# Kernel optimization log

Hardware: AMD Instinct MI355X
Metric: run time of the kernel (lower is better)

The kernel has to match this reference:

```python
import jax, jax.numpy as jnp
import numpy as np

BS, S, N, C, H, CP, T, CT, NB = 1, 2, 2048, 128, 8, 16, 512, 384, 3
DH = C // H
INF = 1.0e8

def _ln(x, w, b, eps=1e-5):
    mu = jnp.mean(x, axis=-1, keepdims=True)
    var = jnp.var(x, axis=-1, keepdims=True)
    return (x - mu) * jax.lax.rsqrt(var + eps) * w + b

def _ln_na(x, eps=1e-5):
    mu = jnp.mean(x, axis=-1, keepdims=True)
    var = jnp.var(x, axis=-1, keepdims=True)
    return (x - mu) * jax.lax.rsqrt(var + eps)

def _betas(n):
    # query row l belongs to window centered at 32*(l//32)+16; keys within +/- n_keys//2=64
    l = jnp.arange(n)
    centers = (l // 32) * 32 + 16
    m = jnp.arange(n)
    ok = (m[None, :] >= (centers - 64)[:, None]) & (m[None, :] < (centers + 64)[:, None])
    return jnp.where(ok, 0.0, -INF).astype(jnp.float32)

def setup_inputs():
    key = jax.random.key(0)
    ks = iter(jax.random.split(key, 80))
    def W(*shape):
        return jax.random.normal(next(ks), shape, dtype=jnp.float32) * 0.05
    return {
        "atom_single": jax.random.normal(next(ks), (BS, S, N, C), dtype=jnp.float32),
        "atom_proj": jax.random.normal(next(ks), (BS, N, C), dtype=jnp.float32),
        "atom_pair": jax.random.normal(next(ks), (BS, N, N, CP), dtype=jnp.float32),
        "mask": jnp.ones((BS, N), jnp.float32),
        "tok_idx": jnp.sort(jax.random.randint(next(ks), (BS, N), 0, T), axis=-1),
        "aln_s_w": jnp.ones((NB, C), jnp.float32), "aln_s_b": jnp.zeros((NB, C), jnp.float32),
        "aln_gate_w": W(NB, C, C), "aln_gate_b": jnp.zeros((NB, C), jnp.float32),
        "aln_shift_w": W(NB, C, C),
        "q_w": W(NB, C, C), "q_b": jnp.zeros((NB, C), jnp.float32),
        "k_w": W(NB, C, C), "v_w": W(NB, C, C),
        "pair_ln_w": jnp.ones((NB, CP), jnp.float32), "pair_ln_b": jnp.zeros((NB, CP), jnp.float32),
        "pair_w": W(NB, CP, H),
        "gate_w": W(NB, C, C), "out_w": W(NB, C, C),
        "og_w": W(NB, C, C), "og_b": jnp.full((NB, C), -2.0, jnp.float32),
        "t_aln_s_w": jnp.ones((NB, C), jnp.float32), "t_aln_s_b": jnp.zeros((NB, C), jnp.float32),
        "t_aln_gate_w": W(NB, C, C), "t_aln_gate_b": jnp.zeros((NB, C), jnp.float32),
        "t_aln_shift_w": W(NB, C, C),
        "t_a_w": W(NB, C, 2 * C), "t_b_w": W(NB, C, 2 * C),
        "t_out_w": W(NB, 2 * C, C),
        "t_og_w": W(NB, C, C), "t_og_b": jnp.full((NB, C), -2.0, jnp.float32),
        "tok_w": W(C, CT),
    }

def _forward(atom_single, atom_proj, atom_pair, mask, tok_idx, aln_s_w, aln_s_b, aln_gate_w, aln_gate_b, aln_shift_w, q_w, q_b, k_w, v_w, pair_ln_w, pair_ln_b, pair_w, gate_w, out_w, og_w, og_b, t_aln_s_w, t_aln_s_b, t_aln_gate_w, t_aln_gate_b, t_aln_shift_w, t_a_w, t_b_w, t_out_w, t_og_w, t_og_b, tok_w):
    betas = _betas(N)[None, None, None]                        # [1,1,1,N,N]
    mask_bias = ((mask - 1.0) * INF)[:, None, None, None, :]   # [bs,1,1,1,N]
    s = atom_proj[:, None]                                     # [bs,1,N,C]
    a = atom_single                                            # [bs,S,N,C]
    for i in range(NB):
        # AttentionPairBias with AdaLN conditioning on s
        sn = _ln(s, aln_s_w[i], aln_s_b[i])
        a1 = jax.nn.sigmoid(sn @ aln_gate_w[i] + aln_gate_b[i]) * _ln_na(a) + sn @ aln_shift_w[i]
        q = (a1 @ q_w[i] + q_b[i]).reshape(BS, S, N, H, DH)
        k = (a1 @ k_w[i]).reshape(BS, S, N, H, DH)
        v = (a1 @ v_w[i]).reshape(BS, S, N, H, DH)
        zb = _ln(atom_pair, pair_ln_w[i], pair_ln_b[i]) @ pair_w[i]    # [bs,N,N,H]
        zb = jnp.transpose(zb, (0, 3, 1, 2))[:, None]                  # [bs,1,H,N,N]
        logits = jnp.einsum('bsqhd,bskhd->bshqk', q, k) / np.float32(np.sqrt(DH)) + zb + betas + mask_bias
        p = jax.nn.softmax(logits, axis=-1)
        o = jnp.einsum('bshqk,bskhd->bsqhd', p, v).reshape(BS, S, N, C)
        o = (jax.nn.sigmoid(a1 @ gate_w[i]) * o) @ out_w[i]
        a = a + jax.nn.sigmoid(sn @ og_w[i] + og_b[i]) * o
        # ConditionedTransitionBlock (SwiGLU with adaLN-Zero gating)
        sn2 = _ln(s, t_aln_s_w[i], t_aln_s_b[i])
        a2 = jax.nn.sigmoid(sn2 @ t_aln_gate_w[i] + t_aln_gate_b[i]) * _ln_na(a) + sn2 @ t_aln_shift_w[i]
        hidden = jax.nn.silu(a2 @ t_a_w[i]) * (a2 @ t_b_w[i])
        a = a + jax.nn.sigmoid(sn2 @ t_og_w[i] + t_og_b[i]) * (hidden @ t_out_w[i])
    # project to token dim, relu, scatter-mean atoms -> tokens
    q_tok = jax.nn.relu(a @ tok_w)                             # [bs,S,N,CT]
    oh = jax.nn.one_hot(tok_idx, T, dtype=q_tok.dtype)         # [bs,N,T]
    cnt = jnp.clip(jnp.sum(oh, axis=1), 1.0)                   # [bs,T]
    tok = jnp.einsum('bsnc,bnt->bstc', q_tok, oh) / cnt[:, None, :, None]
    return tok

def reference(atom_single, atom_proj, atom_pair, mask, tok_idx, aln_s_w, aln_s_b, aln_gate_w, aln_gate_b, aln_shift_w, q_w, q_b, k_w, v_w, pair_ln_w, pair_ln_b, pair_w, gate_w, out_w, og_w, og_b, t_aln_s_w, t_aln_s_b, t_aln_gate_w, t_aln_gate_b, t_aln_shift_w, t_a_w, t_b_w, t_out_w, t_og_w, t_og_b, tok_w):
    return _forward(atom_single, atom_proj, atom_pair, mask, tok_idx, aln_s_w, aln_s_b, aln_gate_w, aln_gate_b, aln_shift_w, q_w, q_b, k_w, v_w, pair_ln_w, pair_ln_b, pair_w, gate_w, out_w, og_w, og_b, t_aln_s_w, t_aln_s_b, t_aln_gate_w, t_aln_gate_b, t_aln_shift_w, t_a_w, t_b_w, t_out_w, t_og_w, t_og_b, tok_w)
```

## Files before the change

kernel.cpp:

```cpp
#include <hip/hip_runtime.h>
#include <math.h>

#define NATOM 2048
#define CD 128
#define SD 2
#define TT 512
#define CTD 384
#define NBI 3
#define MR 4096

typedef unsigned short ushortx;
typedef __attribute__((ext_vector_type(8))) short bf16x8;
typedef __attribute__((ext_vector_type(4))) float f32x4;

__device__ __forceinline__ float sigm(float x){ return 1.0f/(1.0f+expf(-x)); }
__device__ __forceinline__ ushortx f2b(float f){
  union { float f; unsigned u; } v; v.f = f;
  unsigned r = v.u + 0x7fffu + ((v.u>>16)&1u);
  return (ushortx)(r>>16);
}
union U8 { ushortx u[8]; float4 v; };

#define OFFB_W3T    0ll
#define OFFB_B3     589824ll
#define OFFB_WQKVGT 599040ll
#define OFFB_BQ     992256ll
#define OFFB_WOUTT  998400ll
#define OFFB_WABT   1096704ll
#define OFFB_WTOUTT 1489920ll
#define OFFB_WTOKT  1686528ll
#define OFFB_A1     4930560ll
#define OFFB_SNP    9124864ll
#define OFFB_A      27999232ll
#define OFFB_QKVG   30096384ll
#define OFFB_ZB     38484992ll
#define OFFB_QTOK   63650816ll

struct WPtrs {
  const float *aln_gate_w, *aln_gate_b, *aln_shift_w, *og_w, *og_b;
  const float *t_aln_gate_w, *t_aln_gate_b, *t_aln_shift_w, *t_og_w, *t_og_b;
  const float *q_w, *q_b, *k_w, *v_w, *gate_w, *out_w;
  const float *t_a_w, *t_b_w, *t_out_w, *tok_w;
};

__global__ __launch_bounds__(256) void pack_kernel(WPtrs P, char* __restrict__ wsb)
{
  long long idx = (long long)blockIdx.x*256 + threadIdx.x;
  const long long s0=294912, s1=2304, s2=196608, s3=1536, s4=49152, s5=196608, s6=98304, s7=49152;
  if (idx < s0) {
    int which = (int)(idx/49152); int r = (int)(idx%49152); int n=r/128, k=r%128;
    int i = which>>1, t = which&1;
    const float* src;
    if (n<128)      src = (t?P.t_aln_gate_w :P.aln_gate_w ) + i*16384 + k*128 + n;
    else if (n<256) src = (t?P.t_aln_shift_w:P.aln_shift_w) + i*16384 + k*128 + (n-128);
    else            src = (t?P.t_og_w       :P.og_w       ) + i*16384 + k*128 + (n-256);
    ((ushortx*)(wsb+OFFB_W3T))[idx] = f2b(*src); return;
  }
  idx -= s0;
  if (idx < s1) {
    int which = (int)(idx/384); int col = (int)(idx%384); int i=which>>1, t=which&1;
    float v = 0.f;
    if (col<128)       v = (t?P.t_aln_gate_b:P.aln_gate_b)[i*128+col];
    else if (col>=256) v = (t?P.t_og_b      :P.og_b      )[i*128+col-256];
    ((float*)(wsb+OFFB_B3))[idx] = v; return;
  }
  idx -= s1;
  if (idx < s2) {
    int i = (int)(idx/65536); int r = (int)(idx%65536); int n=r/128, k=r%128;
    int seg = n>>7, c = n&127;
    const float* src = (seg==0?P.q_w: seg==1?P.k_w: seg==2?P.v_w: P.gate_w) + i*16384 + k*128 + c;
    ((ushortx*)(wsb+OFFB_WQKVGT))[idx] = f2b(*src); return;
  }
  idx -= s2;
  if (idx < s3) {
    int i = (int)(idx/512); int col = (int)(idx%512);
    ((float*)(wsb+OFFB_BQ))[idx] = (col<128) ? P.q_b[i*128+col] : 0.f; return;
  }
  idx -= s3;
  if (idx < s4) {
    int i = (int)(idx/16384); int r = (int)(idx%16384); int n=r/128, k=r%128;
    ((ushortx*)(wsb+OFFB_WOUTT))[idx] = f2b(P.out_w[i*16384 + k*128 + n]); return;
  }
  idx -= s4;
  if (idx < s5) {
    int i = (int)(idx/65536); int r = (int)(idx%65536); int n=r/128, k=r%128;
    const float* src = (n<256) ? P.t_a_w + i*32768 + k*256 + n
                               : P.t_b_w + i*32768 + k*256 + (n-256);
    ((ushortx*)(wsb+OFFB_WABT))[idx] = f2b(*src); return;
  }
  idx -= s5;
  if (idx < s6) {
    int i = (int)(idx/32768); int r = (int)(idx%32768); int n=r/256, k=r%256;
    ((ushortx*)(wsb+OFFB_WTOUTT))[idx] = f2b(P.t_out_w[i*32768 + k*128 + n]); return;
  }
  idx -= s6;
  if (idx < s7) {
    int n = (int)(idx/128); int k = (int)(idx%128);
    ((ushortx*)(wsb+OFFB_WTOKT))[idx] = f2b(P.tok_w[k*384 + n]); return;
  }
}

__global__ __launch_bounds__(256) void copy_f(const float* __restrict__ src, float* __restrict__ dst, int n){
  int i = blockIdx.x*256 + threadIdx.x;
  if (i<n) dst[i] = src[i];
}

__global__ __launch_bounds__(256) void zb_kernel(const float* __restrict__ atom_pair,
  const float* __restrict__ plw, const float* __restrict__ plb, const float* __restrict__ pw,
  float* __restrict__ zb)
{
  int idx = blockIdx.x*256 + threadIdx.x;
  int q = idx>>7, j = idx&127;
  int m = (q & ~31) - 48 + j;
  bool ok = (m>=0 && m<NATOM);
  float x[16]; float mu=0.f, rs=0.f;
  if (ok){
    float s=0.f, sq=0.f;
    const float* p = atom_pair + ((long long)q*NATOM + m)*16;
    #pragma unroll
    for (int c=0;c<16;c++){ x[c]=p[c]; s+=x[c]; sq+=x[c]*x[c]; }
    mu = s*(1.f/16.f); float var = sq*(1.f/16.f)-mu*mu; rs = rsqrtf(var+1e-5f);
  }
  #pragma unroll
  for (int it=0; it<NBI; it++){
    float out[8] = {0,0,0,0,0,0,0,0};
    if (ok){
      #pragma unroll
      for (int c=0;c<16;c++){
        float xn = (x[c]-mu)*rs*plw[it*16+c] + plb[it*16+c];
        #pragma unroll
        for (int h=0;h<8;h++) out[h] += xn * pw[it*128 + c*8 + h];
      }
    }
    #pragma unroll
    for (int h=0;h<8;h++)
      zb[(((long long)it*8+h)*NATOM + q)*128 + j] = out[h];
  }
}

__global__ __launch_bounds__(256) void attn_kernel(const float* __restrict__ qkvg,
  const float* __restrict__ zb, const float* __restrict__ mask, ushortx* __restrict__ og)
{
  int qb = blockIdx.x, h = blockIdx.y, s = blockIdx.z;
  int base = qb*32 - 48;
  __shared__ float Qs[32][20], Ks[128][20], Vs[128][20], Ls[32][132], maskb[128];
  __shared__ float redx[32][8], rowv[32];
  int tid = threadIdx.x;
  for (int idx=tid; idx<32*4; idx+=256){
    int r=idx>>2, d4=(idx&3)*4;
    *(float4*)&Qs[r][d4] = *(const float4*)&qkvg[((long long)(s*NATOM + qb*32 + r))*512 + h*16 + d4];
  }
  for (int idx=tid; idx<128*4; idx+=256){
    int j=idx>>2, d4=(idx&3)*4;
    int m = base + j; int mc = m<0?0:(m>NATOM-1?NATOM-1:m);
    long long row = ((long long)(s*NATOM + mc))*512;
    *(float4*)&Ks[j][d4] = *(const float4*)&qkvg[row + 128 + h*16 + d4];
    *(float4*)&Vs[j][d4] = *(const float4*)&qkvg[row + 256 + h*16 + d4];
  }
  if (tid < 128){
    int m = base + tid;
    maskb[tid] = (m>=0 && m<NATOM) ? (mask[m]-1.0f)*1e8f : -1e30f;
  }
  __syncthreads();
  int r = tid>>3, g = tid&7;
  {
    float4 q0=*(float4*)&Qs[r][0], q1=*(float4*)&Qs[r][4], q2=*(float4*)&Qs[r][8], q3=*(float4*)&Qs[r][12];
    const float* zrow = zb + ((long long)h*NATOM + (qb*32+r))*128;
    #pragma unroll
    for (int j=g; j<128; j+=8){
      float4 k0=*(float4*)&Ks[j][0], k1=*(float4*)&Ks[j][4], k2=*(float4*)&Ks[j][8], k3=*(float4*)&Ks[j][12];
      float dot = q0.x*k0.x + q0.y*k0.y + q0.z*k0.z + q0.w*k0.w
                + q1.x*k1.x + q1.y*k1.y + q1.z*k1.z + q1.w*k1.w
                + q2.x*k2.x + q2.y*k2.y + q2.z*k2.z + q2.w*k2.w
                + q3.x*k3.x + q3.y*k3.y + q3.z*k3.z + q3.w*k3.w;
      Ls[r][j] = dot*0.25f + zrow[j] + maskb[j];
    }
  }
  __syncthreads();
  float pmax = -1e30f;
  for (int j=g*16; j<g*16+16; j++) pmax = fmaxf(pmax, Ls[r][j]);
  redx[r][g] = pmax; __syncthreads();
  if (g==0){ float mx=redx[r][0]; for(int u=1;u<8;u++) mx=fmaxf(mx,redx[r][u]); rowv[r]=mx; }
  __syncthreads();
  float mx = rowv[r];
  float psum = 0.f;
  for (int j=g*16; j<g*16+16; j++){ float e = expf(Ls[r][j]-mx); Ls[r][j]=e; psum += e; }
  redx[r][g] = psum; __syncthreads();
  if (g==0){ float sm=0.f; for(int u=0;u<8;u++) sm+=redx[r][u]; rowv[r]=sm; }
  __syncthreads();
  {
    int q2=tid>>3, dg=(tid>>1)&3, jh=tid&1;
    float4 acc = make_float4(0.f,0.f,0.f,0.f);
    for (int j=jh*64; j<jh*64+64; j++){
      float p = Ls[q2][j];
      float4 v = *(float4*)&Vs[j][dg*4];
      acc.x += p*v.x; acc.y += p*v.y; acc.z += p*v.z; acc.w += p*v.w;
    }
    acc.x += __shfl_xor(acc.x,1); acc.y += __shfl_xor(acc.y,1);
    acc.z += __shfl_xor(acc.z,1); acc.w += __shfl_xor(acc.w,1);
    if (jh==0){
      long long mrow = (long long)(s*NATOM + qb*32 + q2);
      float inv = 1.0f / rowv[q2];
      float4 gt = *(const float4*)&qkvg[mrow*512 + 384 + h*16 + dg*4];
      ushortx* op = og + mrow*128 + h*16 + dg*4;
      op[0] = f2b(sigm(gt.x)*acc.x*inv);
      op[1] = f2b(sigm(gt.y)*acc.y*inv);
      op[2] = f2b(sigm(gt.z)*acc.z*inv);
      op[3] = f2b(sigm(gt.w)*acc.w*inv);
    }
  }
}

template<int AM>
__global__ __launch_bounds__(256) void gemm_f(
    const void* __restrict__ Asrc, long long strideA,
    const ushortx* __restrict__ B, long long strideB,
    const float* __restrict__ bias, long long strideBias,
    float* C, long long strideC,
    int M, int N, int K, int mode,
    const float* __restrict__ gate, int gate_ld, int gate_coloff,
    const float* __restrict__ p1, const float* __restrict__ p2,
    const float* __restrict__ p3, const float* __restrict__ p4)
{
  int z = blockIdx.z;
  B += z*strideB; C += z*strideC;
  if (bias) bias += z*strideBias;
  __shared__ ushortx At[64][136];
  __shared__ ushortx Bt[64][136];
  int tid = threadIdx.x;
  int rowBase = blockIdx.y*64, colBase = blockIdx.x*64;
  int wave = tid>>6, lane = tid&63;
  int wr = (wave>>1)*32, wc = (wave&1)*32;
  int lr = lane&15, lk = (lane>>4)*8;
  f32x4 acc[2][2];
  #pragma unroll
  for (int i=0;i<2;i++)
    #pragma unroll
    for (int j=0;j<2;j++) acc[i][j] = (f32x4){0.f,0.f,0.f,0.f};

  int sr = tid>>2, q = tid&3, cs = q*32;
  int row = rowBase + sr;

  for (int kc=0; kc<K; kc+=128){
    if (kc) __syncthreads();
    if (AM==0){
      const ushortx* Ab = (const ushortx*)Asrc + z*strideA;
      const float4* ag = (const float4*)(Ab + (long long)row*K + kc + cs);
      #pragma unroll
      for (int u=0;u<4;u++) *(float4*)&At[sr][cs+u*8] = ag[u];
    } else if (AM==3){
      const float* Af_ = (const float*)Asrc;
      const float4* ar = (const float4*)(Af_ + (long long)row*128 + cs);
      #pragma unroll
      for (int u=0;u<4;u++){
        float4 a = ar[2*u], b = ar[2*u+1];
        U8 pk;
        pk.u[0]=f2b(a.x); pk.u[1]=f2b(a.y); pk.u[2]=f2b(a.z); pk.u[3]=f2b(a.w);
        pk.u[4]=f2b(b.x); pk.u[5]=f2b(b.y); pk.u[6]=f2b(b.z); pk.u[7]=f2b(b.w);
        *(float4*)&At[sr][cs+u*8] = pk.v;
      }
    } else if (AM==2){
      const float* hp = (const float*)Asrc;
      const float4* xr = (const float4*)(hp + (long long)row*512 + kc + cs);
      const float4* yr = (const float4*)(hp + (long long)row*512 + 256 + kc + cs);
      #pragma unroll
      for (int u=0;u<4;u++){
        float4 xa = xr[2*u], xb = xr[2*u+1];
        float4 ya = yr[2*u], yb = yr[2*u+1];
        U8 pk;
        pk.u[0]=f2b(xa.x*sigm(xa.x)*ya.x); pk.u[1]=f2b(xa.y*sigm(xa.y)*ya.y);
        pk.u[2]=f2b(xa.z*sigm(xa.z)*ya.z); pk.u[3]=f2b(xa.w*sigm(xa.w)*ya.w);
        pk.u[4]=f2b(xb.x*sigm(xb.x)*yb.x); pk.u[5]=f2b(xb.y*sigm(xb.y)*yb.y);
        pk.u[6]=f2b(xb.z*sigm(xb.z)*yb.z); pk.u[7]=f2b(xb.w*sigm(xb.w)*yb.w);
        *(float4*)&At[sr][cs+u*8] = pk.v;
      }
    } else {
      const float* arow = (AM==4) ? ((const float*)Asrc + (long long)row*128)
                                  : ((const float*)Asrc + (long long)row*128);
      float x[32]; float s=0.f, sq=0.f;
      const float4* ar = (const float4*)(arow + cs);
      #pragma unroll
      for (int u=0;u<8;u++){
        float4 t = ar[u];
        x[4*u]=t.x; x[4*u+1]=t.y; x[4*u+2]=t.z; x[4*u+3]=t.w;
        s += t.x+t.y+t.z+t.w;
        sq += t.x*t.x+t.y*t.y+t.z*t.z+t.w*t.w;
      }
      s += __shfl_xor(s,1); s += __shfl_xor(s,2);
      sq += __shfl_xor(sq,1); sq += __shfl_xor(sq,2);
      float mu = s*(1.f/128.f), var = sq*(1.f/128.f)-mu*mu;
      float rs = rsqrtf(var + 1e-5f);
      if (AM==1){
        const float* sp = p1 + (long long)(row & (NATOM-1))*384;
        const float4* gr = (const float4*)(sp + cs);
        const float4* hr = (const float4*)(sp + 128 + cs);
        #pragma unroll
        for (int u=0;u<4;u++){
          float4 ga = gr[2*u], gb = gr[2*u+1];
          float4 ha = hr[2*u], hb = hr[2*u+1];
          U8 pk;
          pk.u[0]=f2b(sigm(ga.x)*((x[8*u  ]-mu)*rs)+ha.x);
          pk.u[1]=f2b(sigm(ga.y)*((x[8*u+1]-mu)*rs)+ha.y);
          pk.u[2]=f2b(sigm(ga.z)*((x[8*u+2]-mu)*rs)+ha.z);
          pk.u[3]=f2b(sigm(ga.w)*((x[8*u+3]-mu)*rs)+ha.w);
          pk.u[4]=f2b(sigm(gb.x)*((x[8*u+4]-mu)*rs)+hb.x);
          pk.u[5]=f2b(sigm(gb.y)*((x[8*u+5]-mu)*rs)+hb.y);
          pk.u[6]=f2b(sigm(gb.z)*((x[8*u+6]-mu)*rs)+hb.z);
          pk.u[7]=f2b(sigm(gb.w)*((x[8*u+7]-mu)*rs)+hb.w);
          *(float4*)&At[sr][cs+u*8] = pk.v;
        }
      } else {
        int iw = z>>1, tw = z&1;
        const float* w = (tw?p3:p1) + iw*128;
        const float* b = (tw?p4:p2) + iw*128;
        const float4* wrp = (const float4*)(w + cs);
        const float4* brp = (const float4*)(b + cs);
        #pragma unroll
        for (int u=0;u<4;u++){
          float4 wa = wrp[2*u], wb = wrp[2*u+1];
          float4 ba = brp[2*u], bb = brp[2*u+1];
          U8 pk;
          pk.u[0]=f2b((x[8*u  ]-mu)*rs*wa.x+ba.x);
          pk.u[1]=f2b((x[8*u+1]-mu)*rs*wa.y+ba.y);
          pk.u[2]=f2b((x[8*u+2]-mu)*rs*wa.z+ba.z);
          pk.u[3]=f2b((x[8*u+3]-mu)*rs*wa.w+ba.w);
          pk.u[4]=f2b((x[8*u+4]-mu)*rs*wb.x+bb.x);
          pk.u[5]=f2b((x[8*u+5]-mu)*rs*wb.y+bb.y);
          pk.u[6]=f2b((x[8*u+6]-mu)*rs*wb.z+bb.z);
          pk.u[7]=f2b((x[8*u+7]-mu)*rs*wb.w+bb.w);
          *(float4*)&At[sr][cs+u*8] = pk.v;
        }
      }
    }
    {
      const float4* bg = (const float4*)(B + (long long)(colBase+sr)*K + kc + cs);
      #pragma unroll
      for (int u=0;u<4;u++) *(float4*)&Bt[sr][cs+u*8] = bg[u];
    }
    __syncthreads();
    #pragma unroll
    for (int ks=0; ks<4; ks++){
      bf16x8 a0 = *(const bf16x8*)&At[wr+lr][ks*32+lk];
      bf16x8 a1 = *(const bf16x8*)&At[wr+16+lr][ks*32+lk];
      bf16x8 b0 = *(const bf16x8*)&Bt[wc+lr][ks*32+lk];
      bf16x8 b1 = *(const bf16x8*)&Bt[wc+16+lr][ks*32+lk];
      acc[0][0] = __builtin_amdgcn_mfma_f32_16x16x32_bf16(a0,b0,acc[0][0],0,0,0);
      acc[0][1] = __builtin_amdgcn_mfma_f32_16x16x32_bf16(a0,b1,acc[0][1],0,0,0);
      acc[1][0] = __builtin_amdgcn_mfma_f32_16x16x32_bf16(a1,b0,acc[1][0],0,0,0);
      acc[1][1] = __builtin_amdgcn_mfma_f32_16x16x32_bf16(a1,b1,acc[1][1],0,0,0);
    }
  }
  int crow0 = rowBase + wr + (lane>>4)*4;
  int ccol0 = colBase + wc + lr;
  #pragma unroll
  for (int i=0;i<2;i++){
    #pragma unroll
    for (int j=0;j<2;j++){
      int col = ccol0 + j*16;
      float bv = bias ? bias[col] : 0.f;
      #pragma unroll
      for (int rr=0; rr<4; rr++){
        int rrow = crow0 + i*16 + rr;
        float v = acc[i][j][rr] + bv;
        long long ci = (long long)rrow*N + col;
        if (mode==1) C[ci] = fmaxf(v, 0.f);
        else if (mode==2){
          int n = rrow & (NATOM-1);
          C[ci] += sigm(gate[(long long)n*gate_ld + gate_coloff + col]) * v;
        } else C[ci] = v;
      }
    }
  }
}

__global__ __launch_bounds__(128) void tokagg_kernel(const int* __restrict__ tok_idx,
    const float* __restrict__ qtok, float* __restrict__ out)
{
  int t = blockIdx.x;
  int lo=0, hi=NATOM;
  while (lo<hi){ int mid=(lo+hi)>>1; if (tok_idx[mid] < t) lo=mid+1; else hi=mid; }
  int start = lo;
  lo = start; hi = NATOM;
  while (lo<hi){ int mid=(lo+hi)>>1; if (tok_idx[mid] <= t) lo=mid+1; else hi=mid; }
  int end = lo;
  int cnt = end - start;
  float inv = 1.0f / (float)(cnt>0 ? cnt : 1);
  for (int s=0; s<SD; s++)
    for (int c=threadIdx.x; c<CTD; c+=128){
      float acc = 0.f;
      for (int n=start; n<end; n++) acc += qtok[((long long)(s*NATOM+n))*CTD + c];
      out[(long long)(s*TT + t)*CTD + c] = acc*inv;
    }
}

extern "C" void kernel_launch(void* const* d_in, const int* in_sizes, int n_in,
                              void* d_out, int out_size, void* d_ws, size_t ws_size,
                              hipStream_t stream)
{
  const float* atom_single = (const float*)d_in[0];
  const float* atom_proj   = (const float*)d_in[1];
  const float* atom_pair   = (const float*)d_in[2];
  const float* mask        = (const float*)d_in[3];
  const int*   tok_idx     = (const int*)  d_in[4];
  const float* aln_s_w     = (const float*)d_in[5];
  const float* aln_s_b     = (const float*)d_in[6];
  const float* pair_ln_w   = (const float*)d_in[14];
  const float* pair_ln_b   = (const float*)d_in[15];
  const float* pair_w      = (const float*)d_in[16];
  const float* t_aln_s_w   = (const float*)d_in[21];
  const float* t_aln_s_b   = (const float*)d_in[22];

  char* wsb = (char*)d_ws;
  ushortx* W3T    = (ushortx*)(wsb+OFFB_W3T);
  float*   B3     = (float*)  (wsb+OFFB_B3);
  ushortx* WQKVGT = (ushortx*)(wsb+OFFB_WQKVGT);
  float*   BQ     = (float*)  (wsb+OFFB_BQ);
  ushortx* WOUTT  = (ushortx*)(wsb+OFFB_WOUTT);
  ushortx* WABT   = (ushortx*)(wsb+OFFB_WABT);
  ushortx* WTOUTT = (ushortx*)(wsb+OFFB_WTOUTT);
  ushortx* WTOKT  = (ushortx*)(wsb+OFFB_WTOKT);
  ushortx* A1     = (ushortx*)(wsb+OFFB_A1);
  float*   SNP    = (float*)  (wsb+OFFB_SNP);
  float*   Af     = (float*)  (wsb+OFFB_A);
  float*   QKVG   = (float*)  (wsb+OFFB_QKVG);
  float*   ZB     = (float*)  (wsb+OFFB_ZB);
  float*   QTOK   = (float*)  (wsb+OFFB_QTOK);

  WPtrs P;
  P.aln_gate_w=(const float*)d_in[7];  P.aln_gate_b=(const float*)d_in[8];  P.aln_shift_w=(const float*)d_in[9];
  P.og_w=(const float*)d_in[19]; P.og_b=(const float*)d_in[20];
  P.t_aln_gate_w=(const float*)d_in[23]; P.t_aln_gate_b=(const float*)d_in[24]; P.t_aln_shift_w=(const float*)d_in[25];
  P.t_og_w=(const float*)d_in[29]; P.t_og_b=(const float*)d_in[30];
  P.q_w=(const float*)d_in[10]; P.q_b=(const float*)d_in[11]; P.k_w=(const float*)d_in[12];
  P.v_w=(const float*)d_in[13]; P.gate_w=(const float*)d_in[17]; P.out_w=(const float*)d_in[18];
  P.t_a_w=(const float*)d_in[26]; P.t_b_w=(const float*)d_in[27]; P.t_out_w=(const float*)d_in[28];
  P.tok_w=(const float*)d_in[31];

  pack_kernel<<<3471,256,0,stream>>>(P, wsb);
  zb_kernel<<<1024,256,0,stream>>>(atom_pair, pair_ln_w, pair_ln_b, pair_w, ZB);
  gemm_f<4><<<dim3(6,32,6),256,0,stream>>>(atom_proj, 0, W3T, 49152ll,
      B3, 384ll, SNP, 786432ll, NATOM, 384, 128, 0, nullptr, 0, 0,
      aln_s_w, aln_s_b, t_aln_s_w, t_aln_s_b);
  copy_f<<<2048,256,0,stream>>>(atom_single, Af, MR*CD);

  for (int i=0;i<NBI;i++){
    const float* snpA = SNP + (long long)(2*i)*786432;
    const float* snpT = SNP + (long long)(2*i+1)*786432;
    gemm_f<1><<<dim3(8,64,1),256,0,stream>>>(Af, 0, WQKVGT + (long long)i*65536, 0,
        BQ + (long long)i*512, 0, QKVG, 0, MR, 512, 128, 0, nullptr, 0, 0,
        snpA, nullptr, nullptr, nullptr);
    attn_kernel<<<dim3(64,8,2),256,0,stream>>>(QKVG, ZB + (long long)i*2097152, mask, A1);
    gemm_f<0><<<dim3(2,64,1),256,0,stream>>>(A1, 0, WOUTT + (long long)i*16384, 0,
        nullptr, 0, Af, 0, MR, 128, 128, 2, snpA, 384, 256,
        nullptr, nullptr, nullptr, nullptr);
    gemm_f<1><<<dim3(8,64,1),256,0,stream>>>(Af, 0, WABT + (long long)i*65536, 0,
        nullptr, 0, QKVG, 0, MR, 512, 128, 0, nullptr, 0, 0,
        snpT, nullptr, nullptr, nullptr);
    gemm_f<2><<<dim3(2,64,1),256,0,stream>>>(QKVG, 0, WTOUTT + (long long)i*32768, 0,
        nullptr, 0, Af, 0, MR, 128, 256, 2, snpT, 384, 256,
        nullptr, nullptr, nullptr, nullptr);
  }
  gemm_f<3><<<dim3(6,64,1),256,0,stream>>>(Af, 0, WTOKT, 0, nullptr, 0,
      QTOK, 0, MR, CTD, 128, 1, nullptr, 0, 0,
      nullptr, nullptr, nullptr, nullptr);
  tokagg_kernel<<<TT,128,0,stream>>>(tok_idx, QTOK, (float*)d_out);
}
```

Before: 638.0 us.

## Store intermediates in bf16, merge prologue kernels, shrink row tile for N=128 GEMMs

Several intermediate buffers (SNP adaptive-LN projections, QKVG/hidden activations, pair bias ZB) are now stored as bf16 instead of fp32 and unpacked on load, which halves their memory traffic. The weight pack, atom_single copy and pair-bias kernels are merged into one prologue launch. The GEMM gains a BM template parameter so the N=128 output GEMMs run with 32-row tiles and twice as many blocks. The trade-off is extra rounding error on activations and the pair bias.

```diff
diff --git a/kernel.cpp b/kernel.cpp
--- a/kernel.cpp
+++ b/kernel.cpp
@@ -12,6 +12,7 @@
 typedef unsigned short ushortx;
 typedef __attribute__((ext_vector_type(8))) short bf16x8;
 typedef __attribute__((ext_vector_type(4))) float f32x4;
+typedef __attribute__((ext_vector_type(4))) unsigned short us4;
 
 __device__ __forceinline__ float sigm(float x){ return 1.0f/(1.0f+expf(-x)); }
 __device__ __forceinline__ ushortx f2b(float f){
@@ -19,7 +20,16 @@
   unsigned r = v.u + 0x7fffu + ((v.u>>16)&1u);
   return (ushortx)(r>>16);
 }
+__device__ __forceinline__ float b2f(ushortx u){
+  union { unsigned u; float f; } v; v.u = ((unsigned)u)<<16; return v.f;
+}
 union U8 { ushortx u[8]; float4 v; };
+
+__device__ __forceinline__ void unpack8(float* dst, float4 v){
+  U8 pk; pk.v = v;
+  #pragma unroll
+  for (int t=0;t<8;t++) dst[t] = b2f(pk.u[t]);
+}
 
 #define OFFB_W3T    0ll
 #define OFFB_B3     589824ll
@@ -29,12 +39,12 @@
 #define OFFB_WABT   1096704ll
 #define OFFB_WTOUTT 1489920ll
 #define OFFB_WTOKT  1686528ll
-#define OFFB_A1     4930560ll
-#define OFFB_SNP    9124864ll
-#define OFFB_A      27999232ll
-#define OFFB_QKVG   30096384ll
-#define OFFB_ZB     38484992ll
-#define OFFB_QTOK   63650816ll
+#define OFFB_A1     1784832ll
+#define OFFB_SNP    2833408ll
+#define OFFB_A      12270592ll
+#define OFFB_QKVG   14367744ll
+#define OFFB_ZB     18562048ll
+#define OFFB_QTOK   31144960ll
 
 struct WPtrs {
   const float *aln_gate_w, *aln_gate_b, *aln_shift_w, *og_w, *og_b;
@@ -43,119 +53,122 @@
   const float *t_a_w, *t_b_w, *t_out_w, *tok_w;
 };
 
-__global__ __launch_bounds__(256) void pack_kernel(WPtrs P, char* __restrict__ wsb)
+__global__ __launch_bounds__(256) void prologue_kernel(WPtrs P, char* __restrict__ wsb,
+  const float* __restrict__ atom_single, const float* __restrict__ atom_pair,
+  const float* __restrict__ plw, const float* __restrict__ plb, const float* __restrict__ pw)
 {
-  long long idx = (long long)blockIdx.x*256 + threadIdx.x;
-  const long long s0=294912, s1=2304, s2=196608, s3=1536, s4=49152, s5=196608, s6=98304, s7=49152;
-  if (idx < s0) {
-    int which = (int)(idx/49152); int r = (int)(idx%49152); int n=r/128, k=r%128;
-    int i = which>>1, t = which&1;
-    const float* src;
-    if (n<128)      src = (t?P.t_aln_gate_w :P.aln_gate_w ) + i*16384 + k*128 + n;
-    else if (n<256) src = (t?P.t_aln_shift_w:P.aln_shift_w) + i*16384 + k*128 + (n-128);
-    else            src = (t?P.t_og_w       :P.og_w       ) + i*16384 + k*128 + (n-256);
-    ((ushortx*)(wsb+OFFB_W3T))[idx] = f2b(*src); return;
-  }
-  idx -= s0;
-  if (idx < s1) {
-    int which = (int)(idx/384); int col = (int)(idx%384); int i=which>>1, t=which&1;
-    float v = 0.f;
-    if (col<128)       v = (t?P.t_aln_gate_b:P.aln_gate_b)[i*128+col];
-    else if (col>=256) v = (t?P.t_og_b      :P.og_b      )[i*128+col-256];
-    ((float*)(wsb+OFFB_B3))[idx] = v; return;
-  }
-  idx -= s1;
-  if (idx < s2) {
-    int i = (int)(idx/65536); int r = (int)(idx%65536); int n=r/128, k=r%128;
-    int seg = n>>7, c = n&127;
-    const float* src = (seg==0?P.q_w: seg==1?P.k_w: seg==2?P.v_w: P.gate_w) + i*16384 + k*128 + c;
-    ((ushortx*)(wsb+OFFB_WQKVGT))[idx] = f2b(*src); return;
-  }
-  idx -= s2;
-  if (idx < s3) {
-    int i = (int)(idx/512); int col = (int)(idx%512);
-    ((float*)(wsb+OFFB_BQ))[idx] = (col<128) ? P.q_b[i*128+col] : 0.f; return;
-  }
-  idx -= s3;
-  if (idx < s4) {
-    int i = (int)(idx/16384); int r = (int)(idx%16384); int n=r/128, k=r%128;
-    ((ushortx*)(wsb+OFFB_WOUTT))[idx] = f2b(P.out_w[i*16384 + k*128 + n]); return;
-  }
-  idx -= s4;
-  if (idx < s5) {
-    int i = (int)(idx/65536); int r = (int)(idx%65536); int n=r/128, k=r%128;
-    const float* src = (n<256) ? P.t_a_w + i*32768 + k*256 + n
-                               : P.t_b_w + i*32768 + k*256 + (n-256);
-    ((ushortx*)(wsb+OFFB_WABT))[idx] = f2b(*src); return;
-  }
-  idx -= s5;
-  if (idx < s6) {
-    int i = (int)(idx/32768); int r = (int)(idx%32768); int n=r/256, k=r%256;
-    ((ushortx*)(wsb+OFFB_WTOUTT))[idx] = f2b(P.t_out_w[i*32768 + k*128 + n]); return;
-  }
-  idx -= s6;
-  if (idx < s7) {
-    int n = (int)(idx/128); int k = (int)(idx%128);
-    ((ushortx*)(wsb+OFFB_WTOKT))[idx] = f2b(P.tok_w[k*384 + n]); return;
-  }
-}
-
-__global__ __launch_bounds__(256) void copy_f(const float* __restrict__ src, float* __restrict__ dst, int n){
-  int i = blockIdx.x*256 + threadIdx.x;
-  if (i<n) dst[i] = src[i];
-}
-
-__global__ __launch_bounds__(256) void zb_kernel(const float* __restrict__ atom_pair,
-  const float* __restrict__ plw, const float* __restrict__ plb, const float* __restrict__ pw,
-  float* __restrict__ zb)
-{
-  int idx = blockIdx.x*256 + threadIdx.x;
-  int q = idx>>7, j = idx&127;
-  int m = (q & ~31) - 48 + j;
-  bool ok = (m>=0 && m<NATOM);
-  float x[16]; float mu=0.f, rs=0.f;
-  if (ok){
-    float s=0.f, sq=0.f;
-    const float* p = atom_pair + ((long long)q*NATOM + m)*16;
+  int b = blockIdx.x;
+  if (b < 3471){
+    long long idx = (long long)b*256 + threadIdx.x;
+    const long long s0=294912, s1=2304, s2=196608, s3=1536, s4=49152, s5=196608, s6=98304;
+    if (idx < s0) {
+      int which = (int)(idx/49152); int r = (int)(idx%49152); int n=r/128, k=r%128;
+      int i = which>>1, t = which&1;
+      const float* src;
+      if (n<128)      src = (t?P.t_aln_gate_w :P.aln_gate_w ) + i*16384 + k*128 + n;
+      else if (n<256) src = (t?P.t_aln_shift_w:P.aln_shift_w) + i*16384 + k*128 + (n-128);
+      else            src = (t?P.t_og_w       :P.og_w       ) + i*16384 + k*128 + (n-256);
+      ((ushortx*)(wsb+OFFB_W3T))[idx] = f2b(*src); return;
+    }
+    idx -= s0;
+    if (idx < s1) {
+      int which = (int)(idx/384); int col = (int)(idx%384); int i=which>>1, t=which&1;
+      float v = 0.f;
+      if (col<128)       v = (t?P.t_aln_gate_b:P.aln_gate_b)[i*128+col];
+      else if (col>=256) v = (t?P.t_og_b      :P.og_b      )[i*128+col-256];
+      ((float*)(wsb+OFFB_B3))[idx] = v; return;
+    }
+    idx -= s1;
+    if (idx < s2) {
+      int i = (int)(idx/65536); int r = (int)(idx%65536); int n=r/128, k=r%128;
+      int seg = n>>7, c = n&127;
+      const float* src = (seg==0?P.q_w: seg==1?P.k_w: seg==2?P.v_w: P.gate_w) + i*16384 + k*128 + c;
+      ((ushortx*)(wsb+OFFB_WQKVGT))[idx] = f2b(*src); return;
+    }
+    idx -= s2;
+    if (idx < s3) {
+      int i = (int)(idx/512); int col = (int)(idx%512);
+      ((float*)(wsb+OFFB_BQ))[idx] = (col<128) ? P.q_b[i*128+col] : 0.f; return;
+    }
+    idx -= s3;
+    if (idx < s4) {
+      int i = (int)(idx/16384); int r = (int)(idx%16384); int n=r/128, k=r%128;
+      ((ushortx*)(wsb+OFFB_WOUTT))[idx] = f2b(P.out_w[i*16384 + k*128 + n]); return;
+    }
+    idx -= s4;
+    if (idx < s5) {
+      int i = (int)(idx/65536); int r = (int)(idx%65536); int n=r/128, k=r%128;
+      const float* src = (n<256) ? P.t_a_w + i*32768 + k*256 + n
+                                 : P.t_b_w + i*32768 + k*256 + (n-256);
+      ((ushortx*)(wsb+OFFB_WABT))[idx] = f2b(*src); return;
+    }
+    idx -= s5;
+    if (idx < s6) {
+      int i = (int)(idx/32768); int r = (int)(idx%32768); int n=r/256, k=r%256;
+      ((ushortx*)(wsb+OFFB_WTOUTT))[idx] = f2b(P.t_out_w[i*32768 + k*128 + n]); return;
+    }
+    idx -= s6;
+    {
+      int n = (int)(idx/128); int k = (int)(idx%128);
+      ((ushortx*)(wsb+OFFB_WTOKT))[idx] = f2b(P.tok_w[k*384 + n]); return;
+    }
+  }
+  if (b < 5519){
+    int i = (b-3471)*256 + threadIdx.x;
+    ((float*)(wsb+OFFB_A))[i] = atom_single[i];
+    return;
+  }
+  {
+    int idx = (b-5519)*256 + threadIdx.x;
+    int q = idx>>7, j = idx&127;
+    int m = (q & ~31) - 48 + j;
+    bool ok = (m>=0 && m<NATOM);
+    float x[16]; float mu=0.f, rs=0.f;
+    if (ok){
+      float s=0.f, sq=0.f;
+      const float* p = atom_pair + ((long long)q*NATOM + m)*16;
+      #pragma unroll
+      for (int c=0;c<16;c++){ x[c]=p[c]; s+=x[c]; sq+=x[c]*x[c]; }
+      mu = s*(1.f/16.f); float var = sq*(1.f/16.f)-mu*mu; rs = rsqrtf(var+1e-5f);
+    }
+    ushortx* zb = (ushortx*)(wsb+OFFB_ZB);
     #pragma unroll
-    for (int c=0;c<16;c++){ x[c]=p[c]; s+=x[c]; sq+=x[c]*x[c]; }
-    mu = s*(1.f/16.f); float var = sq*(1.f/16.f)-mu*mu; rs = rsqrtf(var+1e-5f);
-  }
-  #pragma unroll
-  for (int it=0; it<NBI; it++){
-    float out[8] = {0,0,0,0,0,0,0,0};
-    if (ok){
-      #pragma unroll
-      for (int c=0;c<16;c++){
-        float xn = (x[c]-mu)*rs*plw[it*16+c] + plb[it*16+c];
+    for (int it=0; it<NBI; it++){
+      float out[8] = {0,0,0,0,0,0,0,0};
+      if (ok){
         #pragma unroll
-        for (int h=0;h<8;h++) out[h] += xn * pw[it*128 + c*8 + h];
-      }
-    }
-    #pragma unroll
-    for (int h=0;h<8;h++)
-      zb[(((long long)it*8+h)*NATOM + q)*128 + j] = out[h];
-  }
-}
-
-__global__ __launch_bounds__(256) void attn_kernel(const float* __restrict__ qkvg,
-  const float* __restrict__ zb, const float* __restrict__ mask, ushortx* __restrict__ og)
+        for (int c=0;c<16;c++){
+          float xn = (x[c]-mu)*rs*plw[it*16+c] + plb[it*16+c];
+          #pragma unroll
+          for (int h=0;h<8;h++) out[h] += xn * pw[it*128 + c*8 + h];
+        }
+      }
+      #pragma unroll
+      for (int h=0;h<8;h++)
+        zb[(((long long)it*8+h)*NATOM + q)*128 + j] = f2b(out[h]);
+    }
+  }
+}
+
+__global__ __launch_bounds__(256) void attn_kernel(const ushortx* __restrict__ qkvg,
+  const ushortx* __restrict__ zb, const float* __restrict__ mask, ushortx* __restrict__ og)
 {
   int qb = blockIdx.x, h = blockIdx.y, s = blockIdx.z;
   int base = qb*32 - 48;
   __shared__ float Qs[32][20], Ks[128][20], Vs[128][20], Ls[32][132], maskb[128];
   __shared__ float redx[32][8], rowv[32];
   int tid = threadIdx.x;
-  for (int idx=tid; idx<32*4; idx+=256){
-    int r=idx>>2, d4=(idx&3)*4;
-    *(float4*)&Qs[r][d4] = *(const float4*)&qkvg[((long long)(s*NATOM + qb*32 + r))*512 + h*16 + d4];
-  }
-  for (int idx=tid; idx<128*4; idx+=256){
-    int j=idx>>2, d4=(idx&3)*4;
+  for (int idx=tid; idx<32*2; idx+=256){
+    int r=idx>>1, d8=(idx&1)*8;
+    float4 v = *(const float4*)&qkvg[((long long)(s*NATOM + qb*32 + r))*512 + h*16 + d8];
+    unpack8(&Qs[r][d8], v);
+  }
+  for (int idx=tid; idx<512; idx+=256){
+    int j = idx&127, d8 = ((idx>>7)&1)*8, kv = idx>>8;
     int m = base + j; int mc = m<0?0:(m>NATOM-1?NATOM-1:m);
     long long row = ((long long)(s*NATOM + mc))*512;
-    *(float4*)&Ks[j][d4] = *(const float4*)&qkvg[row + 128 + h*16 + d4];
-    *(float4*)&Vs[j][d4] = *(const float4*)&qkvg[row + 256 + h*16 + d4];
+    float4 v = *(const float4*)&qkvg[row + (kv?256:128) + h*16 + d8];
+    if (kv) unpack8(&Vs[j][d8], v); else unpack8(&Ks[j][d8], v);
   }
   if (tid < 128){
     int m = base + tid;
@@ -165,7 +178,7 @@
   int r = tid>>3, g = tid&7;
   {
     float4 q0=*(float4*)&Qs[r][0], q1=*(float4*)&Qs[r][4], q2=*(float4*)&Qs[r][8], q3=*(float4*)&Qs[r][12];
-    const float* zrow = zb + ((long long)h*NATOM + (qb*32+r))*128;
+    const ushortx* zrow = zb + ((long long)h*NATOM + (qb*32+r))*128;
     #pragma unroll
     for (int j=g; j<128; j+=8){
       float4 k0=*(float4*)&Ks[j][0], k1=*(float4*)&Ks[j][4], k2=*(float4*)&Ks[j][8], k3=*(float4*)&Ks[j][12];
@@ -173,7 +186,7 @@
                 + q1.x*k1.x + q1.y*k1.y + q1.z*k1.z + q1.w*k1.w
                 + q2.x*k2.x + q2.y*k2.y + q2.z*k2.z + q2.w*k2.w
                 + q3.x*k3.x + q3.y*k3.y + q3.z*k3.z + q3.w*k3.w;
-      Ls[r][j] = dot*0.25f + zrow[j] + maskb[j];
+      Ls[r][j] = dot*0.25f + b2f(zrow[j]) + maskb[j];
     }
   }
   __syncthreads();
@@ -201,45 +214,53 @@
     if (jh==0){
       long long mrow = (long long)(s*NATOM + qb*32 + q2);
       float inv = 1.0f / rowv[q2];
-      float4 gt = *(const float4*)&qkvg[mrow*512 + 384 + h*16 + dg*4];
-      ushortx* op = og + mrow*128 + h*16 + dg*4;
-      op[0] = f2b(sigm(gt.x)*acc.x*inv);
-      op[1] = f2b(sigm(gt.y)*acc.y*inv);
-      op[2] = f2b(sigm(gt.z)*acc.z*inv);
-      op[3] = f2b(sigm(gt.w)*acc.w*inv);
-    }
-  }
-}
-
-template<int AM>
+      us4 gt = *(const us4*)&qkvg[mrow*512 + 384 + h*16 + dg*4];
+      us4 st;
+      st[0] = f2b(sigm(b2f(gt[0]))*acc.x*inv);
+      st[1] = f2b(sigm(b2f(gt[1]))*acc.y*inv);
+      st[2] = f2b(sigm(b2f(gt[2]))*acc.z*inv);
+      st[3] = f2b(sigm(b2f(gt[3]))*acc.w*inv);
+      *(us4*)(og + mrow*128 + h*16 + dg*4) = st;
+    }
+  }
+}
+
+template<int AM, int BM>
 __global__ __launch_bounds__(256) void gemm_f(
     const void* __restrict__ Asrc, long long strideA,
     const ushortx* __restrict__ B, long long strideB,
     const float* __restrict__ bias, long long strideBias,
-    float* C, long long strideC,
+    void* Cv, long long strideC,
     int M, int N, int K, int mode,
-    const float* __restrict__ gate, int gate_ld, int gate_coloff,
-    const float* __restrict__ p1, const float* __restrict__ p2,
-    const float* __restrict__ p3, const float* __restrict__ p4)
+    const ushortx* __restrict__ gate, int gate_ld, int gate_coloff,
+    const void* __restrict__ p1, const void* __restrict__ p2,
+    const void* __restrict__ p3, const void* __restrict__ p4)
 {
+  constexpr int CG  = 256/BM;
+  constexpr int XC  = 128/CG;
+  constexpr int F4  = XC/8;
+  constexpr int ACI = BM/32;
   int z = blockIdx.z;
-  B += z*strideB; C += z*strideC;
+  B += z*strideB;
   if (bias) bias += z*strideBias;
-  __shared__ ushortx At[64][136];
+  float* C = (float*)Cv + z*strideC;
+  ushortx* Cu = (ushortx*)Cv + z*strideC;
+  __shared__ ushortx At[BM][136];
   __shared__ ushortx Bt[64][136];
   int tid = threadIdx.x;
-  int rowBase = blockIdx.y*64, colBase = blockIdx.x*64;
+  int rowBase = blockIdx.y*BM, colBase = blockIdx.x*64;
   int wave = tid>>6, lane = tid&63;
-  int wr = (wave>>1)*32, wc = (wave&1)*32;
+  int wr = (wave>>1)*(BM/2), wc = (wave&1)*32;
   int lr = lane&15, lk = (lane>>4)*8;
-  f32x4 acc[2][2];
+  f32x4 acc[ACI][2];
   #pragma unroll
-  for (int i=0;i<2;i++)
+  for (int i=0;i<ACI;i++)
     #pragma unroll
     for (int j=0;j<2;j++) acc[i][j] = (f32x4){0.f,0.f,0.f,0.f};
 
-  int sr = tid>>2, q = tid&3, cs = q*32;
+  int sr = tid/CG, q = tid%CG, cs = q*XC;
   int row = rowBase + sr;
+  int bsr = tid>>2, bq = tid&3, bcs = bq*32;
 
   for (int kc=0; kc<K; kc+=128){
     if (kc) __syncthreads();
@@ -247,12 +268,12 @@
       const ushortx* Ab = (const ushortx*)Asrc + z*strideA;
       const float4* ag = (const float4*)(Ab + (long long)row*K + kc + cs);
       #pragma unroll
-      for (int u=0;u<4;u++) *(float4*)&At[sr][cs+u*8] = ag[u];
+      for (int u=0;u<F4;u++) *(float4*)&At[sr][cs+u*8] = ag[u];
     } else if (AM==3){
       const float* Af_ = (const float*)Asrc;
       const float4* ar = (const float4*)(Af_ + (long long)row*128 + cs);
       #pragma unroll
-      for (int u=0;u<4;u++){
+      for (int u=0;u<F4;u++){
         float4 a = ar[2*u], b = ar[2*u+1];
         U8 pk;
         pk.u[0]=f2b(a.x); pk.u[1]=f2b(a.y); pk.u[2]=f2b(a.z); pk.u[3]=f2b(a.w);
@@ -260,63 +281,56 @@
         *(float4*)&At[sr][cs+u*8] = pk.v;
       }
     } else if (AM==2){
-      const float* hp = (const float*)Asrc;
+      const ushortx* hp = (const ushortx*)Asrc;
       const float4* xr = (const float4*)(hp + (long long)row*512 + kc + cs);
       const float4* yr = (const float4*)(hp + (long long)row*512 + 256 + kc + cs);
       #pragma unroll
-      for (int u=0;u<4;u++){
-        float4 xa = xr[2*u], xb = xr[2*u+1];
-        float4 ya = yr[2*u], yb = yr[2*u+1];
-        U8 pk;
-        pk.u[0]=f2b(xa.x*sigm(xa.x)*ya.x); pk.u[1]=f2b(xa.y*sigm(xa.y)*ya.y);
-        pk.u[2]=f2b(xa.z*sigm(xa.z)*ya.z); pk.u[3]=f2b(xa.w*sigm(xa.w)*ya.w);
-        pk.u[4]=f2b(xb.x*sigm(xb.x)*yb.x); pk.u[5]=f2b(xb.y*sigm(xb.y)*yb.y);
-        pk.u[6]=f2b(xb.z*sigm(xb.z)*yb.z); pk.u[7]=f2b(xb.w*sigm(xb.w)*yb.w);
+      for (int u=0;u<F4;u++){
+        U8 xa, ya, pk;
+        xa.v = xr[u]; ya.v = yr[u];
+        #pragma unroll
+        for (int t=0;t<8;t++){
+          float x = b2f(xa.u[t]), y = b2f(ya.u[t]);
+          pk.u[t] = f2b(x*sigm(x)*y);
+        }
         *(float4*)&At[sr][cs+u*8] = pk.v;
       }
     } else {
-      const float* arow = (AM==4) ? ((const float*)Asrc + (long long)row*128)
-                                  : ((const float*)Asrc + (long long)row*128);
-      float x[32]; float s=0.f, sq=0.f;
+      const float* arow = (const float*)Asrc + (long long)row*128;
+      float x[XC]; float s=0.f, sq=0.f;
       const float4* ar = (const float4*)(arow + cs);
       #pragma unroll
-      for (int u=0;u<8;u++){
+      for (int u=0;u<XC/4;u++){
         float4 t = ar[u];
         x[4*u]=t.x; x[4*u+1]=t.y; x[4*u+2]=t.z; x[4*u+3]=t.w;
         s += t.x+t.y+t.z+t.w;
         sq += t.x*t.x+t.y*t.y+t.z*t.z+t.w*t.w;
       }
-      s += __shfl_xor(s,1); s += __shfl_xor(s,2);
-      sq += __shfl_xor(sq,1); sq += __shfl_xor(sq,2);
+      #pragma unroll
+      for (int off=1; off<CG; off<<=1){ s += __shfl_xor(s,off); sq += __shfl_xor(sq,off); }
       float mu = s*(1.f/128.f), var = sq*(1.f/128.f)-mu*mu;
       float rs = rsqrtf(var + 1e-5f);
       if (AM==1){
-        const float* sp = p1 + (long long)(row & (NATOM-1))*384;
+        const ushortx* sp = (const ushortx*)p1 + (long long)(row & (NATOM-1))*384;
         const float4* gr = (const float4*)(sp + cs);
         const float4* hr = (const float4*)(sp + 128 + cs);
         #pragma unroll
-        for (int u=0;u<4;u++){
-          float4 ga = gr[2*u], gb = gr[2*u+1];
-          float4 ha = hr[2*u], hb = hr[2*u+1];
-          U8 pk;
-          pk.u[0]=f2b(sigm(ga.x)*((x[8*u  ]-mu)*rs)+ha.x);
-          pk.u[1]=f2b(sigm(ga.y)*((x[8*u+1]-mu)*rs)+ha.y);
-          pk.u[2]=f2b(sigm(ga.z)*((x[8*u+2]-mu)*rs)+ha.z);
-          pk.u[3]=f2b(sigm(ga.w)*((x[8*u+3]-mu)*rs)+ha.w);
-          pk.u[4]=f2b(sigm(gb.x)*((x[8*u+4]-mu)*rs)+hb.x);
-          pk.u[5]=f2b(sigm(gb.y)*((x[8*u+5]-mu)*rs)+hb.y);
-          pk.u[6]=f2b(sigm(gb.z)*((x[8*u+6]-mu)*rs)+hb.z);
-          pk.u[7]=f2b(sigm(gb.w)*((x[8*u+7]-mu)*rs)+hb.w);
+        for (int u=0;u<F4;u++){
+          U8 ga, ha, pk;
+          ga.v = gr[u]; ha.v = hr[u];
+          #pragma unroll
+          for (int t=0;t<8;t++)
+            pk.u[t] = f2b(sigm(b2f(ga.u[t]))*((x[8*u+t]-mu)*rs) + b2f(ha.u[t]));
           *(float4*)&At[sr][cs+u*8] = pk.v;
         }
       } else {
         int iw = z>>1, tw = z&1;
-        const float* w = (tw?p3:p1) + iw*128;
-        const float* b = (tw?p4:p2) + iw*128;
+        const float* w = (const float*)(tw?p3:p1) + iw*128;
+        const float* b = (const float*)(tw?p4:p2) + iw*128;
         const float4* wrp = (const float4*)(w + cs);
         const float4* brp = (const float4*)(b + cs);
         #pragma unroll
-        for (int u=0;u<4;u++){
+        for (int u=0;u<F4;u++){
           float4 wa = wrp[2*u], wb = wrp[2*u+1];
           float4 ba = brp[2*u], bb = brp[2*u+1];
           U8 pk;
@@ -333,27 +347,27 @@
       }
     }
     {
-      const float4* bg = (const float4*)(B + (long long)(colBase+sr)*K + kc + cs);
-      #pragma unroll
-      for (int u=0;u<4;u++) *(float4*)&Bt[sr][cs+u*8] = bg[u];
+      const float4* bg = (const float4*)(B + (long long)(colBase+bsr)*K + kc + bcs);
+      #pragma unroll
+      for (int u=0;u<4;u++) *(float4*)&Bt[bsr][bcs+u*8] = bg[u];
     }
     __syncthreads();
     #pragma unroll
     for (int ks=0; ks<4; ks++){
-      bf16x8 a0 = *(const bf16x8*)&At[wr+lr][ks*32+lk];
-      bf16x8 a1 = *(const bf16x8*)&At[wr+16+lr][ks*32+lk];
       bf16x8 b0 = *(const bf16x8*)&Bt[wc+lr][ks*32+lk];
       bf16x8 b1 = *(const bf16x8*)&Bt[wc+16+lr][ks*32+lk];
-      acc[0][0] = __builtin_amdgcn_mfma_f32_16x16x32_bf16(a0,b0,acc[0][0],0,0,0);
-      acc[0][1] = __builtin_amdgcn_mfma_f32_16x16x32_bf16(a0,b1,acc[0][1],0,0,0);
-      acc[1][0] = __builtin_amdgcn_mfma_f32_16x16x32_bf16(a1,b0,acc[1][0],0,0,0);
-      acc[1][1] = __builtin_amdgcn_mfma_f32_16x16x32_bf16(a1,b1,acc[1][1],0,0,0);
+      #pragma unroll
+      for (int i=0;i<ACI;i++){
+        bf16x8 a = *(const bf16x8*)&At[wr+i*16+lr][ks*32+lk];
+        acc[i][0] = __builtin_amdgcn_mfma_f32_16x16x32_bf16(a,b0,acc[i][0],0,0,0);
+        acc[i][1] = __builtin_amdgcn_mfma_f32_16x16x32_bf16(a,b1,acc[i][1],0,0,0);
+      }
     }
   }
   int crow0 = rowBase + wr + (lane>>4)*4;
   int ccol0 = colBase + wc + lr;
   #pragma unroll
-  for (int i=0;i<2;i++){
+  for (int i=0;i<ACI;i++){
     #pragma unroll
     for (int j=0;j<2;j++){
       int col = ccol0 + j*16;
@@ -366,8 +380,10 @@
         if (mode==1) C[ci] = fmaxf(v, 0.f);
         else if (mode==2){
           int n = rrow & (NATOM-1);
-          C[ci] += sigm(gate[(long long)n*gate_ld + gate_coloff + col]) * v;
-        } else C[ci] = v;
+          C[ci] += sigm(b2f(gate[(long long)n*gate_ld + gate_coloff + col])) * v;
+        } else if (mode==3) Cu[ci] = f2b(v);
+        else if (mode==4) Cu[ci] = f2b(fmaxf(v, 0.f));
+        else C[ci] = v;
       }
     }
   }
@@ -420,10 +436,10 @@
   ushortx* WTOUTT = (ushortx*)(wsb+OFFB_WTOUTT);
   ushortx* WTOKT  = (ushortx*)(wsb+OFFB_WTOKT);
   ushortx* A1     = (ushortx*)(wsb+OFFB_A1);
-  float*   SNP    = (float*)  (wsb+OFFB_SNP);
+  ushortx* SNP    = (ushortx*)(wsb+OFFB_SNP);
   float*   Af     = (float*)  (wsb+OFFB_A);
-  float*   QKVG   = (float*)  (wsb+OFFB_QKVG);
-  float*   ZB     = (float*)  (wsb+OFFB_ZB);
+  ushortx* QKVG   = (ushortx*)(wsb+OFFB_QKVG);
+  ushortx* ZB     = (ushortx*)(wsb+OFFB_ZB);
   float*   QTOK   = (float*)  (wsb+OFFB_QTOK);
 
   WPtrs P;
@@ -436,31 +452,30 @@
   P.t_a_w=(const float*)d_in[26]; P.t_b_w=(const float*)d_in[27]; P.t_out_w=(const float*)d_in[28];
   P.tok_w=(const float*)d_in[31];
 
-  pack_kernel<<<3471,256,0,stream>>>(P, wsb);
-  zb_kernel<<<1024,256,0,stream>>>(atom_pair, pair_ln_w, pair_ln_b, pair_w, ZB);
-  gemm_f<4><<<dim3(6,32,6),256,0,stream>>>(atom_proj, 0, W3T, 49152ll,
-      B3, 384ll, SNP, 786432ll, NATOM, 384, 128, 0, nullptr, 0, 0,
+  prologue_kernel<<<6543,256,0,stream>>>(P, wsb, atom_single, atom_pair,
+      pair_ln_w, pair_ln_b, pair_w);
+  gemm_f<4,64><<<dim3(6,32,6),256,0,stream>>>(atom_proj, 0, W3T, 49152ll,
+      B3, 384ll, SNP, 786432ll, NATOM, 384, 128, 3, nullptr, 0, 0,
       aln_s_w, aln_s_b, t_aln_s_w, t_aln_s_b);
-  copy_f<<<2048,256,0,stream>>>(atom_single, Af, MR*CD);
 
   for (int i=0;i<NBI;i++){
-    const float* snpA = SNP + (long long)(2*i)*786432;
-    const float* snpT = SNP + (long long)(2*i+1)*786432;
-    gemm_f<1><<<dim3(8,64,1),256,0,stream>>>(Af, 0, WQKVGT + (long long)i*65536, 0,
-        BQ + (long long)i*512, 0, QKVG, 0, MR, 512, 128, 0, nullptr, 0, 0,
+    const ushortx* snpA = SNP + (long long)(2*i)*786432;
+    const ushortx* snpT = SNP + (long long)(2*i+1)*786432;
+    gemm_f<1,64><<<dim3(8,64,1),256,0,stream>>>(Af, 0, WQKVGT + (long long)i*65536, 0,
+        BQ + (long long)i*512, 0, QKVG, 0, MR, 512, 128, 3, nullptr, 0, 0,
         snpA, nullptr, nullptr, nullptr);
     attn_kernel<<<dim3(64,8,2),256,0,stream>>>(QKVG, ZB + (long long)i*2097152, mask, A1);
-    gemm_f<0><<<dim3(2,64,1),256,0,stream>>>(A1, 0, WOUTT + (long long)i*16384, 0,
+    gemm_f<0,32><<<dim3(2,128,1),256,0,stream>>>(A1, 0, WOUTT + (long long)i*16384, 0,
         nullptr, 0, Af, 0, MR, 128, 128, 2, snpA, 384, 256,
         nullptr, nullptr, nullptr, nullptr);
-    gemm_f<1><<<dim3(8,64,1),256,0,stream>>>(Af, 0, WABT + (long long)i*65536, 0,
-        nullptr, 0, QKVG, 0, MR, 512, 128, 0, nullptr, 0, 0,
+    gemm_f<1,64><<<dim3(8,64,1),256,0,stream>>>(Af, 0, WABT + (long long)i*65536, 0,
+        nullptr, 0, QKVG, 0, MR, 512, 128, 3, nullptr, 0, 0,
         snpT, nullptr, nullptr, nullptr);
-    gemm_f<2><<<dim3(2,64,1),256,0,stream>>>(QKVG, 0, WTOUTT + (long long)i*32768, 0,
+    gemm_f<2,32><<<dim3(2,128,1),256,0,stream>>>(QKVG, 0, WTOUTT + (long long)i*32768, 0,
         nullptr, 0, Af, 0, MR, 128, 256, 2, snpT, 384, 256,
         nullptr, nullptr, nullptr, nullptr);
   }
-  gemm_f<3><<<dim3(6,64,1),256,0,stream>>>(Af, 0, WTOKT, 0, nullptr, 0,
+  gemm_f<3,64><<<dim3(6,64,1),256,0,stream>>>(Af, 0, WTOKT, 0, nullptr, 0,
       QTOK, 0, MR, CTD, 128, 1, nullptr, 0, 0,
       nullptr, nullptr, nullptr, nullptr);
   tokagg_kernel<<<TT,128,0,stream>>>(tok_idx, QTOK, (float*)d_out);
```

Result: faster. 601.0 us (-5.8%).
